# Kernel tuning notes

Measured on AMD Instinct MI355X. Metric: run time of the kernel, lower is better.

## Reference

```python
import jax, jax.numpy as jnp
import numpy as np

DECAY = 0.99


def setup_inputs() -> dict:
    key = jax.random.key(0)
    k1, k2, k3 = jax.random.split(key, 3)
    B, D, H, W = 16, 128, 32, 32
    K = 8192
    z_e = jax.random.normal(k1, (B, D, H, W), dtype=jnp.float32)
    codebook = jax.random.normal(k2, (K, D), dtype=jnp.float32)
    ema_count = jnp.ones((K,), dtype=jnp.float32)
    ema_weight = codebook  # buffer initialized as codebook.clone()
    return {"z_e": z_e, "codebook": codebook, "ema_count": ema_count, "ema_weight": ema_weight}


def reference(z_e, codebook, ema_count, ema_weight):
    B, D, H, W = z_e.shape
    K = codebook.shape[0]
    # (B,D,H,W) -> (N,D)
    z_flat = z_e.transpose(0, 2, 3, 1).reshape(-1, D)
    # squared L2 distances: ||z||^2 - 2 z.C^T + ||C||^2  -> (N,K)
    dist = (
        jnp.sum(z_flat * z_flat, axis=1, keepdims=True)
        - 2.0 * (z_flat @ codebook.T)
        + jnp.sum(codebook * codebook, axis=1)[None, :]
    )
    indices = jnp.argmin(dist, axis=1)  # (N,)
    z_q = codebook[indices].reshape(B, H, W, D).transpose(0, 3, 1, 2)
    # EMA codebook update (training path, no grad)
    counts = jax.ops.segment_sum(jnp.ones_like(indices, dtype=jnp.float32), indices, num_segments=K)
    dw = jax.ops.segment_sum(z_flat, indices, num_segments=K)  # (K,D)
    new_count = ema_count * DECAY + (1.0 - DECAY) * counts
    new_weight = ema_weight * DECAY + (1.0 - DECAY) * dw
    new_codebook = new_weight / jnp.maximum(new_count, 1.0)[:, None]
    # straight-through estimator
    z_q_st = z_e + jax.lax.stop_gradient(z_q - z_e)
    return (z_q_st, indices.reshape(B, H, W), new_codebook, new_count, new_weight)
```

## Files before the change

### kernel.cpp

```cpp
#include <hip/hip_runtime.h>

#define D 128
#define HW 1024
#define NROWS 16384
#define K 8192
#define NU 32

#define OUT0 0
#define OUT1 2097152
#define OUT2 2113536
#define OUT3 3162112
#define OUT4 3170304

typedef __attribute__((ext_vector_type(8))) _Float16 half8;
typedef __attribute__((ext_vector_type(16))) float f32x16;
typedef unsigned short u16;
typedef unsigned long long u64;

__device__ __forceinline__ void gld16(const u16* gsrc, u16* ldst) {
    __builtin_amdgcn_global_load_lds(
        (const __attribute__((address_space(1))) unsigned int*)gsrc,
        (__attribute__((address_space(3))) unsigned int*)ldst,
        16, 0, 0);
}

__global__ __launch_bounds__(256) void k_prep(const float* __restrict__ cb,
                                              u16* __restrict__ Bg,
                                              float* __restrict__ cnorm,
                                              u64* __restrict__ packed,
                                              float* __restrict__ counts,
                                              float* __restrict__ dw) {
    const int tid = threadIdx.x;
    int kk = tid & 15;
    int k = blockIdx.x * 16 + (tid >> 4);
    const float* src = cb + (size_t)k * D + kk * 8;
    half8 h, l;
    float s = 0.f;
#pragma unroll
    for (int j = 0; j < 8; ++j) {
        float v = src[j];
        s += v * v;
        _Float16 hv = (_Float16)v;
        _Float16 lv = (_Float16)(v - (float)hv);
        h[j] = hv;
        l[j] = lv;
    }
    int g = k >> 6, col = k & 63;
    size_t offH = (size_t)g * 16384 + ((size_t)kk * 64 + col) * 8;
    *(half8*)((_Float16*)Bg + offH) = h;
    *(half8*)((_Float16*)Bg + offH + 8192) = l;
#pragma unroll
    for (int off = 8; off > 0; off >>= 1) s += __shfl_down(s, off);
    if (kk == 0) cnorm[k] = s;
    float4 z4 = {0.f, 0.f, 0.f, 0.f};
    size_t zi = ((size_t)blockIdx.x * 256 + tid) * 8;
    *(float4*)(dw + zi) = z4;
    *(float4*)(dw + zi + 4) = z4;
    int gid = blockIdx.x * 256 + tid;
    if (gid < NROWS) packed[gid] = ~0ull;
    if (gid < K) counts[gid] = 0.f;
}

__global__ __launch_bounds__(512, 4) void k_argmin_mfma(
        const float* __restrict__ z_e,
        const u16* __restrict__ Bg,
        const float* __restrict__ cnorm, u64* __restrict__ packed) {
    __shared__ u16 lds[2][16384];

    const int tid = threadIdx.x;
    const int ln  = tid & 63;
    const int l31 = ln & 31;
    const int lh  = ln >> 5;
    const int wv  = tid >> 6;
    const int wy  = wv & 3;
    const int wx  = wv >> 2;

    const int rg = blockIdx.x >> 2;
    const int k0 = (blockIdx.x & 3) * 2048;
    const int g0 = k0 >> 6;

    const int row = (rg * 4 + wy) * 32 + l31;
    const float* zrow = z_e + ((size_t)(row >> 10)) * (D * HW) + (row & 1023);
    half8 Ah[8], Al[8];
#pragma unroll
    for (int ks = 0; ks < 8; ++ks) {
        half8 h, l;
#pragma unroll
        for (int j = 0; j < 8; ++j) {
            float v = zrow[(size_t)(ks * 16 + lh * 8 + j) * HW];
            _Float16 hv = (_Float16)v;
            h[j] = hv;
            l[j] = (_Float16)(v - (float)hv);
        }
        Ah[ks] = h;
        Al[ks] = l;
    }

    {
        const u16* src = Bg + (size_t)g0 * 16384;
#pragma unroll
        for (int r = 0; r < 4; ++r)
            gld16(src + ((size_t)r * 512 + tid) * 8, lds[0] + (r * 512 + tid) * 8);
    }

    float minv[16];
    int   mini[16];
#pragma unroll
    for (int r = 0; r < 16; ++r) { minv[r] = INFINITY; mini[r] = 0; }

#pragma unroll 1
    for (int u = 0; u < NU; ++u) {
        const u16* buf = lds[u & 1];
        const int c0 = k0 + u * 64 + wx * 32 + l31;

        float cn0 = cnorm[c0];

        if (u + 1 < NU) {
            const u16* src = Bg + (size_t)(g0 + u + 1) * 16384;
            u16* dst = lds[(u + 1) & 1];
#pragma unroll
            for (int r = 0; r < 4; ++r)
                gld16(src + ((size_t)r * 512 + tid) * 8, dst + (r * 512 + tid) * 8);
            asm volatile("s_waitcnt vmcnt(4)" ::: "memory");
        } else {
            asm volatile("s_waitcnt vmcnt(0)" ::: "memory");
        }
        asm volatile("s_barrier" ::: "memory");

        f32x16 acc = {};
        const _Float16* bh = (const _Float16*)buf;
        const _Float16* bl = bh + 8192;

#pragma unroll
        for (int ks = 0; ks < 8; ++ks) {
            const int bo = ((ks * 2 + lh) * 64 + wx * 32 + l31) * 8;
            half8 b0 = *(const half8*)(bl + bo);
            acc = __builtin_amdgcn_mfma_f32_32x32x16_f16(Ah[ks], b0, acc, 0, 0, 0);
        }
#pragma unroll
        for (int ks = 0; ks < 8; ++ks) {
            const int bo = ((ks * 2 + lh) * 64 + wx * 32 + l31) * 8;
            half8 b0 = *(const half8*)(bh + bo);
            acc = __builtin_amdgcn_mfma_f32_32x32x16_f16(Ah[ks], b0, acc, 0, 0, 0);
            acc = __builtin_amdgcn_mfma_f32_32x32x16_f16(Al[ks], b0, acc, 0, 0, 0);
        }

#pragma unroll
        for (int r = 0; r < 16; ++r) {
            float d0 = fmaf(-2.0f, acc[r], cn0);
            if (d0 < minv[r]) { minv[r] = d0; mini[r] = c0; }
        }
        asm volatile("s_barrier" ::: "memory");
    }

#pragma unroll
    for (int r = 0; r < 16; ++r) {
        float v = minv[r];
        int ix = mini[r];
#pragma unroll
        for (int off = 1; off < 32; off <<= 1) {
            float v2 = __shfl_xor(v, off);
            int i2 = __shfl_xor(ix, off);
            if (v2 < v || (v2 == v && i2 < ix)) { v = v2; ix = i2; }
        }
        if (l31 == 0) {
            int orow = rg * 128 + wy * 32 + 4 * lh + (r & 3) + 8 * (r >> 2);
            unsigned int uenc = __float_as_uint(v);
            uenc = (uenc & 0x80000000u) ? ~uenc : (uenc | 0x80000000u);
            u64 pk = ((u64)uenc << 13) | (u64)(unsigned)ix;
            atomicMin(&packed[orow], pk);
        }
    }
}

__global__ __launch_bounds__(256) void k_epilogue(const float* __restrict__ z_e,
                                                  const float* __restrict__ cb,
                                                  const u64* __restrict__ packed,
                                                  float* __restrict__ out0,
                                                  float* __restrict__ out1,
                                                  float* __restrict__ counts,
                                                  float* __restrict__ dw) {
    __shared__ float zS[128][33];
    __shared__ float cbS[32][129];
    __shared__ int idxS[32];
    const int tid = threadIdx.x;
    const int n0 = blockIdx.x * 32;
    const int bb = n0 >> 10, p0 = n0 & 1023;

    if (tid < 32) {
        int ix = (int)(packed[n0 + tid] & 0x1FFFull);
        idxS[tid] = ix;
        out1[n0 + tid] = (float)ix;
        atomicAdd(&counts[ix], 1.0f);
    }
    __syncthreads();

    const float* zb = z_e + (size_t)bb * (D * HW) + p0;
    float* ob = out0 + (size_t)bb * (D * HW) + p0;

    for (int i = tid; i < 32 * D; i += 256) {
        int row = i >> 7, d = i & 127;
        cbS[row][d] = cb[(size_t)idxS[row] * D + d];
    }
    for (int i = tid; i < 32 * D; i += 256) {
        int d = i >> 5, r = i & 31;
        zS[d][r] = zb[(size_t)d * HW + r];
    }
    __syncthreads();
    for (int i = tid; i < 32 * D; i += 256) {
        int d = i >> 5, r = i & 31;
        float z = zS[d][r];
        float c = cbS[r][d];
        ob[(size_t)d * HW + r] = z + (c - z);
    }
    for (int i = tid; i < 32 * D; i += 256) {
        int r = i >> 7, d = i & 127;
        atomicAdd(&dw[(size_t)idxS[r] * D + d], zS[d][r]);
    }
}

__global__ __launch_bounds__(256) void k_final(const float* __restrict__ ema_count,
                                               const float* __restrict__ ema_weight,
                                               float* __restrict__ out2,
                                               float* __restrict__ out3,
                                               float* __restrict__ out4) {
    int gid = blockIdx.x * 256 + threadIdx.x;
    int k = gid >> 5, d4 = gid & 31;
    float cnt_raw = out3[k];
    float4 dw4 = *(const float4*)(out4 + (size_t)gid * 4);
    float4 ew4 = *(const float4*)(ema_weight + (size_t)gid * 4);
    float ec = ema_count[k];
    __syncthreads();
    float nc = 0.99f * ec + 0.01f * cnt_raw;
    float den = fmaxf(nc, 1.0f);
    float4 nw, o2;
    nw.x = 0.99f * ew4.x + 0.01f * dw4.x;  o2.x = nw.x / den;
    nw.y = 0.99f * ew4.y + 0.01f * dw4.y;  o2.y = nw.y / den;
    nw.z = 0.99f * ew4.z + 0.01f * dw4.z;  o2.z = nw.z / den;
    nw.w = 0.99f * ew4.w + 0.01f * dw4.w;  o2.w = nw.w / den;
    *(float4*)(out4 + (size_t)gid * 4) = nw;
    *(float4*)(out2 + (size_t)gid * 4) = o2;
    if (d4 == 0) out3[k] = nc;
}

extern "C" void kernel_launch(void* const* d_in, const int* in_sizes, int n_in,
                              void* d_out, int out_size, void* d_ws, size_t ws_size,
                              hipStream_t stream) {
    const float* z_e        = (const float*)d_in[0];
    const float* cb         = (const float*)d_in[1];
    const float* ema_count  = (const float*)d_in[2];
    const float* ema_weight = (const float*)d_in[3];
    float* out = (float*)d_out;

    float* cnorm = (float*)d_ws;
    u64* packed = (u64*)((char*)d_ws + K * 4);

    u16* Bg = (u16*)(out + OUT2);

    k_prep       <<<512,               256, 0, stream>>>(cb, Bg, cnorm,
                                                         packed, out + OUT3, out + OUT4);
    k_argmin_mfma<<<512,               512, 0, stream>>>(z_e, Bg, cnorm, packed);
    k_epilogue   <<<NROWS / 32,        256, 0, stream>>>(z_e, cb, packed,
                                                         out + OUT0, out + OUT1,
                                                         out + OUT3, out + OUT4);
    k_final      <<<(K * D / 4) / 256, 256, 0, stream>>>(ema_count, ema_weight,
                                                         out + OUT2, out + OUT3, out + OUT4);
}
```

Before: 199.9 us.

## Drop LDS staging in argmin kernel; read codebook directly from global

The argmin kernel no longer stages codebook tiles through double-buffered LDS with barriers. Each wave now loads its B fragments straight from global/L2, using 256-thread blocks where each wave covers all 2048 codes of its quarter in 64 steps of 32 columns. The MFMA chain is split into two accumulators to shorten the dependency chain, and the min update uses selects. This removes barrier and LDS overhead but relies on L2/L1 to supply each B tile to four waves, which may raise global traffic and memory latency.

```diff
diff --git a/kernel.cpp b/kernel.cpp
--- a/kernel.cpp
+++ b/kernel.cpp
@@ -4,7 +4,6 @@
 #define HW 1024
 #define NROWS 16384
 #define K 8192
-#define NU 32
 
 #define OUT0 0
 #define OUT1 2097152
@@ -16,13 +15,6 @@
 typedef __attribute__((ext_vector_type(16))) float f32x16;
 typedef unsigned short u16;
 typedef unsigned long long u64;
-
-__device__ __forceinline__ void gld16(const u16* gsrc, u16* ldst) {
-    __builtin_amdgcn_global_load_lds(
-        (const __attribute__((address_space(1))) unsigned int*)gsrc,
-        (__attribute__((address_space(3))) unsigned int*)ldst,
-        16, 0, 0);
-}
 
 __global__ __launch_bounds__(256) void k_prep(const float* __restrict__ cb,
                                               u16* __restrict__ Bg,
@@ -61,25 +53,21 @@
     if (gid < K) counts[gid] = 0.f;
 }
 
-__global__ __launch_bounds__(512, 4) void k_argmin_mfma(
+__global__ __launch_bounds__(256, 2) void k_argmin_mfma(
         const float* __restrict__ z_e,
         const u16* __restrict__ Bg,
         const float* __restrict__ cnorm, u64* __restrict__ packed) {
-    __shared__ u16 lds[2][16384];
-
     const int tid = threadIdx.x;
     const int ln  = tid & 63;
     const int l31 = ln & 31;
     const int lh  = ln >> 5;
-    const int wv  = tid >> 6;
-    const int wy  = wv & 3;
-    const int wx  = wv >> 2;
+    const int wy  = tid >> 6;
 
     const int rg = blockIdx.x >> 2;
     const int k0 = (blockIdx.x & 3) * 2048;
-    const int g0 = k0 >> 6;
-
-    const int row = (rg * 4 + wy) * 32 + l31;
+    const int band = rg * 4 + wy;
+
+    const int row = band * 32 + l31;
     const float* zrow = z_e + ((size_t)(row >> 10)) * (D * HW) + (row & 1023);
     half8 Ah[8], Al[8];
 #pragma unroll
@@ -96,12 +84,7 @@
         Al[ks] = l;
     }
 
-    {
-        const u16* src = Bg + (size_t)g0 * 16384;
-#pragma unroll
-        for (int r = 0; r < 4; ++r)
-            gld16(src + ((size_t)r * 512 + tid) * 8, lds[0] + (r * 512 + tid) * 8);
-    }
+    const _Float16* Bf = (const _Float16*)Bg;
 
     float minv[16];
     int   mini[16];
@@ -109,48 +92,34 @@
     for (int r = 0; r < 16; ++r) { minv[r] = INFINITY; mini[r] = 0; }
 
 #pragma unroll 1
-    for (int u = 0; u < NU; ++u) {
-        const u16* buf = lds[u & 1];
-        const int c0 = k0 + u * 64 + wx * 32 + l31;
-
+    for (int u = 0; u < 64; ++u) {
+        const int c0 = k0 + u * 32 + l31;
         float cn0 = cnorm[c0];
 
-        if (u + 1 < NU) {
-            const u16* src = Bg + (size_t)(g0 + u + 1) * 16384;
-            u16* dst = lds[(u + 1) & 1];
-#pragma unroll
-            for (int r = 0; r < 4; ++r)
-                gld16(src + ((size_t)r * 512 + tid) * 8, dst + (r * 512 + tid) * 8);
-            asm volatile("s_waitcnt vmcnt(4)" ::: "memory");
-        } else {
-            asm volatile("s_waitcnt vmcnt(0)" ::: "memory");
-        }
-        asm volatile("s_barrier" ::: "memory");
-
-        f32x16 acc = {};
-        const _Float16* bh = (const _Float16*)buf;
+        const int g = (k0 >> 6) + (u >> 1);
+        const _Float16* bh = Bf + (size_t)g * 16384 + ((u & 1) * 32 + l31) * 8;
         const _Float16* bl = bh + 8192;
 
+        f32x16 accA = {}, accB = {};
 #pragma unroll
         for (int ks = 0; ks < 8; ++ks) {
-            const int bo = ((ks * 2 + lh) * 64 + wx * 32 + l31) * 8;
-            half8 b0 = *(const half8*)(bl + bo);
-            acc = __builtin_amdgcn_mfma_f32_32x32x16_f16(Ah[ks], b0, acc, 0, 0, 0);
+            half8 b = *(const half8*)(bl + (ks * 2 + lh) * 512);
+            accA = __builtin_amdgcn_mfma_f32_32x32x16_f16(Ah[ks], b, accA, 0, 0, 0);
         }
 #pragma unroll
         for (int ks = 0; ks < 8; ++ks) {
-            const int bo = ((ks * 2 + lh) * 64 + wx * 32 + l31) * 8;
-            half8 b0 = *(const half8*)(bh + bo);
-            acc = __builtin_amdgcn_mfma_f32_32x32x16_f16(Ah[ks], b0, acc, 0, 0, 0);
-            acc = __builtin_amdgcn_mfma_f32_32x32x16_f16(Al[ks], b0, acc, 0, 0, 0);
+            half8 b = *(const half8*)(bh + (ks * 2 + lh) * 512);
+            accB = __builtin_amdgcn_mfma_f32_32x32x16_f16(Ah[ks], b, accB, 0, 0, 0);
+            accA = __builtin_amdgcn_mfma_f32_32x32x16_f16(Al[ks], b, accA, 0, 0, 0);
         }
 
 #pragma unroll
         for (int r = 0; r < 16; ++r) {
-            float d0 = fmaf(-2.0f, acc[r], cn0);
-            if (d0 < minv[r]) { minv[r] = d0; mini[r] = c0; }
-        }
-        asm volatile("s_barrier" ::: "memory");
+            float d0 = fmaf(-2.0f, accA[r] + accB[r], cn0);
+            bool p = d0 < minv[r];
+            minv[r] = p ? d0 : minv[r];
+            mini[r] = p ? c0 : mini[r];
+        }
     }
 
 #pragma unroll
@@ -164,7 +133,7 @@
             if (v2 < v || (v2 == v && i2 < ix)) { v = v2; ix = i2; }
         }
         if (l31 == 0) {
-            int orow = rg * 128 + wy * 32 + 4 * lh + (r & 3) + 8 * (r >> 2);
+            int orow = band * 32 + 4 * lh + (r & 3) + 8 * (r >> 2);
             unsigned int uenc = __float_as_uint(v);
             uenc = (uenc & 0x80000000u) ? ~uenc : (uenc | 0x80000000u);
             u64 pk = ((u64)uenc << 13) | (u64)(unsigned)ix;
@@ -259,7 +228,7 @@
 
     k_prep       <<<512,               256, 0, stream>>>(cb, Bg, cnorm,
                                                          packed, out + OUT3, out + OUT4);
-    k_argmin_mfma<<<512,               512, 0, stream>>>(z_e, Bg, cnorm, packed);
+    k_argmin_mfma<<<512,               256, 0, stream>>>(z_e, Bg, cnorm, packed);
     k_epilogue   <<<NROWS / 32,        256, 0, stream>>>(z_e, cb, packed,
                                                          out + OUT0, out + OUT1,
                                                          out + OUT3, out + OUT4);
```

After: 231.9 us. +16.0%, slower.
